# Kernel optimization log

Hardware: AMD Instinct MI355X
Metric: run time of the kernel (lower is better)

Reference implementation:

```python
import jax, jax.numpy as jnp
import numpy as np

HIDDEN = 4544
NUM_HEADS = 71
HEAD_DIM = 64
ROPE_BASE = 10000.0


def _rope_cos_sin(seq_len, dim, dtype):
    inv_freq = 1.0 / (ROPE_BASE ** (jnp.arange(0, dim, 2, dtype=jnp.float32) / dim))
    t = jnp.arange(seq_len, dtype=jnp.float32)
    freqs = jnp.einsum('i,j->ij', t, inv_freq)            # [S, dim/2]
    emb = jnp.concatenate([freqs, freqs], axis=-1)        # [S, dim]
    return jnp.cos(emb).astype(dtype), jnp.sin(emb).astype(dtype)


def _rotate_half(x):
    half = x.shape[-1] // 2
    return jnp.concatenate([-x[..., half:], x[..., :half]], axis=-1)


def _apply_rope(x, cos, sin):
    # x: [..., S, hd]; cos/sin: [S, hd]
    return x * cos + _rotate_half(x) * sin


def setup_inputs() -> dict:
    key = jax.random.key(0)
    k1, k2, k3 = jax.random.split(key, 3)
    B, S = 1, 1024
    hidden_states = jax.random.normal(k1, (B, 1, S, HIDDEN), dtype=jnp.float32) * 0.02
    # additive causal mask (prefill)
    neg = jnp.triu(jnp.full((S, S), -1e9, dtype=jnp.float32), k=1)
    attention_mask = jnp.broadcast_to(neg[None, None], (B, 1, S, S))
    # fused QKV weight (already transposed for right-matmul): [H, (nh+2)*hd]
    qkv_w = jax.random.normal(k2, (HIDDEN, (NUM_HEADS + 2) * HEAD_DIM), dtype=jnp.float32) * 0.02
    dense_w = jax.random.normal(k3, (HIDDEN, HIDDEN), dtype=jnp.float32) * 0.02
    return {"hidden_states": hidden_states, "attention_mask": attention_mask,
            "qkv_w": qkv_w, "dense_w": dense_w}


def reference(hidden_states, attention_mask, qkv_w, dense_w):
    B, _, S, H = hidden_states.shape
    nh, hd = NUM_HEADS, HEAD_DIM
    x = hidden_states[:, 0]                               # [B, S, H]
    fused = jnp.einsum('bsh,hf->bsf', x, qkv_w)           # [B, S, (nh+2)*hd]
    fused = fused.reshape(B, S, nh + 2, hd)
    q = jnp.transpose(fused[:, :, :nh, :], (0, 2, 1, 3))  # [B, nh, S, hd]
    k = fused[:, :, nh, :]                                # [B, S, hd]  (single KV head, MQA)
    v = fused[:, :, nh + 1, :]                            # [B, S, hd]
    cos, sin = _rope_cos_sin(S, hd, q.dtype)
    q = _apply_rope(q, cos, sin)
    k = _apply_rope(k, cos, sin)
    scale = 1.0 / np.sqrt(hd).astype(np.float32)
    scores = jnp.einsum('bhsd,btd->bhst', q, k) * scale   # [B, nh, S, S]
    scores = scores + attention_mask                      # broadcast over heads
    probs = jax.nn.softmax(scores, axis=-1)
    ctx = jnp.einsum('bhst,btd->bhsd', probs, v)          # [B, nh, S, hd]
    ctx = jnp.transpose(ctx, (0, 2, 1, 3)).reshape(B, S, nh * hd)
    out = jnp.einsum('bsh,hg->bsg', ctx, dense_w)         # [B, S, H]
    return out[:, None]                                   # [B, 1, S, H]
```

## Files before the change

### kernel.cpp

```cpp
#include <hip/hip_runtime.h>

#define S_LEN 1024
#define HID   4544
#define NH    71
#define NQKV  4672
#define NQKV_PAD 4736
#define ND_PAD   4608

typedef __attribute__((ext_vector_type(4)))  float f32x4;
typedef __attribute__((ext_vector_type(4))) unsigned short u16x4;
typedef __attribute__((ext_vector_type(8))) unsigned short u16x8;
typedef __attribute__((ext_vector_type(8))) __bf16 bf16x8;

__device__ __forceinline__ bf16x8 as_bf(u16x8 v) { return __builtin_bit_cast(bf16x8, v); }

__device__ __forceinline__ unsigned short f2bf(float f) {
    unsigned u = __builtin_bit_cast(unsigned, f);
    return (unsigned short)((u + 0x7FFFu + ((u >> 16) & 1u)) >> 16);
}
__device__ __forceinline__ float bf2f(unsigned short u) {
    return __builtin_bit_cast(float, (unsigned)u << 16);
}
__device__ __forceinline__ unsigned pk2(float a, float b) {
    return (unsigned)f2bf(a) | ((unsigned)f2bf(b) << 16);
}
__device__ __forceinline__ void gload16(const void* g, void* l) {
    __builtin_amdgcn_global_load_lds((const __attribute__((address_space(1))) unsigned int*)g,
                                     (__attribute__((address_space(3))) unsigned int*)l,
                                     16, 0, 0);
}

__global__ __launch_bounds__(256) void cvt_x_kernel(const float4* __restrict__ x,
                                                    ushort4* __restrict__ y) {
    int i = blockIdx.x * 256 + threadIdx.x;
    float4 v = x[i];
    ushort4 r;
    r.x = f2bf(v.x); r.y = f2bf(v.y); r.z = f2bf(v.z); r.w = f2bf(v.w);
    y[i] = r;
}

__global__ __launch_bounds__(256) void cvt_wT_kernel(const float* __restrict__ w,
                                                     unsigned short* __restrict__ wt,
                                                     int K, int N) {
    __shared__ float t[64][65];
    int n0 = blockIdx.x * 64, k0 = blockIdx.y * 64;
    int tx = threadIdx.x & 15, ty = threadIdx.x >> 4;
#pragma unroll
    for (int r = 0; r < 64; r += 16) {
        int k = k0 + ty + r;
        int n = n0 + tx * 4;
        float4 v = make_float4(0.f, 0.f, 0.f, 0.f);
        if (n < N) v = *(const float4*)&w[(size_t)k * N + n];
        t[ty + r][tx * 4 + 0] = v.x;
        t[ty + r][tx * 4 + 1] = v.y;
        t[ty + r][tx * 4 + 2] = v.z;
        t[ty + r][tx * 4 + 3] = v.w;
    }
    __syncthreads();
    int nr = threadIdx.x >> 2;
    int kq = (threadIdx.x & 3) * 16;
    unsigned short tmp[16];
#pragma unroll
    for (int z = 0; z < 16; z++) tmp[z] = f2bf(t[kq + z][nr]);
    u16x8* dst = (u16x8*)&wt[(size_t)(n0 + nr) * K + k0 + kq];
    dst[0] = *(const u16x8*)&tmp[0];
    dst[1] = *(const u16x8*)&tmp[8];
}

__global__ void rope_table_kernel(float* __restrict__ cs, float* __restrict__ sn) {
    int s = blockIdx.x, i = threadIdx.x;
    float inv = powf(10000.0f, -(2.0f * (float)i) / 64.0f);
    float f = (float)s * inv;
    cs[s * 32 + i] = cosf(f);
    sn[s * 32 + i] = sinf(f);
}

template<int EPI>
__global__ __launch_bounds__(128, 2) void gemm_bt_kernel(
        const unsigned short* __restrict__ A, const unsigned short* __restrict__ BT,
        void* __restrict__ Cout, const float* __restrict__ cs_t,
        const float* __restrict__ sn_t, unsigned short* __restrict__ k_out,
        unsigned short* __restrict__ v_out, int K, int ldc, int n_store) {
    __shared__ unsigned short As[2][64 * 64];
    __shared__ unsigned short Bs[2][128 * 64];
    int p = blockIdx.x;
    int per = gridDim.x >> 3;
    int l = (p & 7) * per + (p >> 3);
    int msl = l & 15, nb = l >> 4;
    int m0 = msl * 64, n0 = nb * 128;
    int t = threadIdx.x;
    int wn = t >> 6;
    int lane = t & 63, lr = lane & 15, lg = lane >> 4;

    f32x4 acc[4][4];
#pragma unroll
    for (int mi = 0; mi < 4; mi++)
#pragma unroll
        for (int ni = 0; ni < 4; ni++) acc[mi][ni] = (f32x4)0.0f;

    const char* Ab = (const char*)A;
    const char* Bb = (const char*)BT;
    size_t rs = (size_t)K * 2;

    auto stage = [&](int step, int buf) {
        size_t kb = (size_t)step * 128;
#pragma unroll
        for (int i = 0; i < 4; i++) {
            int chunk = i * 128 + t;
            int row = chunk >> 3, c8 = chunk & 7;
            int csrc = c8 ^ (row & 7);
            gload16(Ab + (size_t)(m0 + row) * rs + kb + csrc * 16,
                    (char*)As[buf] + chunk * 16);
        }
#pragma unroll
        for (int i = 0; i < 8; i++) {
            int chunk = i * 128 + t;
            int row = chunk >> 3, c8 = chunk & 7;
            int csrc = c8 ^ (row & 7);
            gload16(Bb + (size_t)(n0 + row) * rs + kb + csrc * 16,
                    (char*)Bs[buf] + chunk * 16);
        }
    };

    int nsteps = K >> 6;
    stage(0, 0);
    if (nsteps > 1) stage(1, 1);
    for (int s = 0; s < nsteps; ++s) {
        int cur = s & 1;
        if (s + 1 < nsteps) { asm volatile("s_waitcnt vmcnt(12)" ::: "memory"); }
        else                { asm volatile("s_waitcnt vmcnt(0)" ::: "memory"); }
        __builtin_amdgcn_s_barrier();
        bf16x8 af[4][2], bfr[4][2];
#pragma unroll
        for (int mi = 0; mi < 4; mi++) {
            int row = mi * 16 + lr;
#pragma unroll
            for (int kk = 0; kk < 2; kk++)
                af[mi][kk] = as_bf(*(const u16x8*)&As[cur][row * 64 + (((kk * 4 + lg) ^ (row & 7)) << 3)]);
        }
#pragma unroll
        for (int ni = 0; ni < 4; ni++) {
            int row = wn * 64 + ni * 16 + lr;
#pragma unroll
            for (int kk = 0; kk < 2; kk++)
                bfr[ni][kk] = as_bf(*(const u16x8*)&Bs[cur][row * 64 + (((kk * 4 + lg) ^ (row & 7)) << 3)]);
        }
        asm volatile("s_waitcnt lgkmcnt(0)" ::: "memory");
        __builtin_amdgcn_s_barrier();
        if (s + 2 < nsteps) stage(s + 2, cur);
#pragma unroll
        for (int kk = 0; kk < 2; kk++)
#pragma unroll
            for (int mi = 0; mi < 4; mi++)
#pragma unroll
                for (int ni = 0; ni < 4; ni++)
                    acc[mi][ni] = __builtin_amdgcn_mfma_f32_16x16x32_bf16(
                        af[mi][kk], bfr[ni][kk], acc[mi][ni], 0, 0, 0);
    }

    if (EPI == 0) {
        float* C = (float*)Cout;
#pragma unroll
        for (int mi = 0; mi < 4; mi++)
#pragma unroll
            for (int ni = 0; ni < 4; ni++) {
                int col = n0 + wn * 64 + ni * 16 + lr;
                if (col < n_store) {
#pragma unroll
                    for (int i = 0; i < 4; i++) {
                        int row = m0 + mi * 16 + 4 * lg + i;
                        C[(size_t)row * ldc + col] = acc[mi][ni][i];
                    }
                }
            }
    } else {
        int hh = nb * 2 + wn;
        if (hh == 72) {
#pragma unroll
            for (int mi = 0; mi < 4; mi++)
#pragma unroll
                for (int ni = 0; ni < 4; ni++) {
                    int d = ni * 16 + lr;
                    int s0 = m0 + mi * 16 + 4 * lg;
                    u16x4 pk;
#pragma unroll
                    for (int i = 0; i < 4; i++) pk[i] = f2bf(acc[mi][ni][i]);
                    *(u16x4*)&v_out[(size_t)d * S_LEN + s0] = pk;
                }
        } else if (hh < 72) {
            unsigned short* qb = (unsigned short*)Cout;
            float qscale = (hh < 71) ? 0.125f : 1.0f;
#pragma unroll
            for (int mi = 0; mi < 4; mi++)
#pragma unroll
                for (int i = 0; i < 4; i++) {
                    int s = m0 + mi * 16 + 4 * lg + i;
                    float c0 = cs_t[s * 32 + lr],      g0 = sn_t[s * 32 + lr];
                    float c1 = cs_t[s * 32 + 16 + lr], g1 = sn_t[s * 32 + 16 + lr];
#pragma unroll
                    for (int ni = 0; ni < 4; ni++) {
                        float x  = acc[mi][ni][i];
                        float xp = acc[mi][ni ^ 2][i];
                        float c = (ni & 1) ? c1 : c0;
                        float g = (ni & 1) ? g1 : g0;
                        float r = (ni < 2) ? (x * c - xp * g) : (x * c + xp * g);
                        r *= qscale;
                        int d = ni * 16 + lr;
                        if (hh < 71) qb[(size_t)s * HID + hh * 64 + d] = f2bf(r);
                        else         k_out[(size_t)s * 64 + d] = f2bf(r);
                    }
                }
        }
    }
}

__global__ __launch_bounds__(256, 3) void attn_kernel(
        const unsigned short* __restrict__ qb, const unsigned short* __restrict__ kr,
        const unsigned short* __restrict__ vt, unsigned short* __restrict__ ctx,
        unsigned short* __restrict__ Opart, float2* __restrict__ MLpart) {
    __shared__ unsigned short Ks[2][64 * 64];
    __shared__ unsigned short Vs[2][64 * 64];
    __shared__ unsigned short Pl[4][16 * 72];
    int h = blockIdx.y;
    int u = blockIdx.x;
    int c, j0;
    if (u < 16)      { c = 0; j0 = u * 4; }
    else if (u < 28) { c = 1; j0 = 16 + (u - 16) * 4; }
    else if (u < 36) { c = 2; j0 = 32 + (u - 28) * 4; }
    else             { c = 3; j0 = 48 + (u - 36) * 4; }
    int t = threadIdx.x, wv = t >> 6, lane = t & 63, lr = lane & 15, lg = lane >> 4;
    int j = j0 + wv;
    int qs = j * 16 + lr;
    int k_lo = c * 256;
    int kend_w   = min((j + 1) * 16, k_lo + 256);
    int kend_max = min((j0 + 4) * 16, k_lo + 256);
    int nt = (kend_max - k_lo) >> 6;
    int nch = (j >> 4) + 1;
    int srow = t >> 3, sc16 = t & 7, sw = lr & 7;

    auto stage = [&](int ti, int buf) {
        size_t kbase = (size_t)(k_lo + ti * 64);
#pragma unroll
        for (int i = 0; i < 2; i++) {
            int row = i * 32 + srow;
            int csrc = sc16 ^ (row & 7);
            gload16((const char*)kr + (kbase + row) * 128 + csrc * 16,
                    (char*)Ks[buf] + (i * 256 + t) * 16);
        }
#pragma unroll
        for (int i = 0; i < 2; i++) {
            int row = i * 32 + srow;
            int csrc = sc16 ^ (row & 7);
            gload16((const char*)vt + (size_t)row * 2048 + kbase * 2 + csrc * 16,
                    (char*)Vs[buf] + (i * 256 + t) * 16);
        }
    };

    bf16x8 qf[2];
#pragma unroll
    for (int dc = 0; dc < 2; dc++)
        qf[dc] = as_bf(*(const u16x8*)&qb[(size_t)qs * HID + h * 64 + dc * 32 + 8 * lg]);

    float m_i = -1e30f, l_i = 0.0f;
    f32x4 o[4];
#pragma unroll
    for (int d4 = 0; d4 < 4; d4++) o[d4] = (f32x4)0.0f;

    stage(0, 0);
    if (nt > 1) stage(1, 1);

    for (int ti = 0; ti < nt; ti++) {
        int cur = ti & 1;
        if (ti + 1 < nt) { asm volatile("s_waitcnt vmcnt(4)" ::: "memory"); }
        else             { asm volatile("s_waitcnt vmcnt(0)" ::: "memory"); }
        __builtin_amdgcn_s_barrier();
        int k0 = k_lo + ti * 64;
        if (k0 < kend_w) {
            f32x4 st[4];
#pragma unroll
            for (int nc = 0; nc < 4; nc++) st[nc] = (f32x4)0.0f;
#pragma unroll
            for (int nc = 0; nc < 4; nc++) {
                int krow = nc * 16 + lr;
#pragma unroll
                for (int dc = 0; dc < 2; dc++) {
                    bf16x8 kf = as_bf(*(const u16x8*)&Ks[cur][krow * 64 + (((dc * 4 + lg) ^ sw) << 3)]);
                    st[nc] = __builtin_amdgcn_mfma_f32_16x16x32_bf16(kf, qf[dc], st[nc], 0, 0, 0);
                }
            }
            bool needmask = (k0 + 64 > j * 16);
            float mx = -1e30f;
            if (needmask) {
#pragma unroll
                for (int nc = 0; nc < 4; nc++)
#pragma unroll
                    for (int i = 0; i < 4; i++) {
                        int ks = k0 + nc * 16 + 4 * lg + i;
                        float v = (ks <= qs) ? st[nc][i] : -1e30f;
                        st[nc][i] = v;
                        mx = fmaxf(mx, v);
                    }
            } else {
#pragma unroll
                for (int nc = 0; nc < 4; nc++)
#pragma unroll
                    for (int i = 0; i < 4; i++) mx = fmaxf(mx, st[nc][i]);
            }
            mx = fmaxf(mx, __shfl_xor(mx, 16));
            mx = fmaxf(mx, __shfl_xor(mx, 32));
            if (!__all(mx <= m_i + 8.0f)) {
                float mn = fmaxf(m_i, mx);
                float so = __expf(m_i - mn);
                l_i *= so;
#pragma unroll
                for (int d4 = 0; d4 < 4; d4++)
#pragma unroll
                    for (int i = 0; i < 4; i++) o[d4][i] *= so;
                m_i = mn;
            }
            float ps = 0.0f;
#pragma unroll
            for (int nc = 0; nc < 4; nc++)
#pragma unroll
                for (int i = 0; i < 4; i++) {
                    float v = st[nc][i];
                    float e = (!needmask || v > -1e29f) ? __expf(v - m_i) : 0.0f;
                    st[nc][i] = e;
                    ps += e;
                }
            ps += __shfl_xor(ps, 16);
            ps += __shfl_xor(ps, 32);
            l_i += ps;
#pragma unroll
            for (int nc = 0; nc < 4; nc++) {
                *(unsigned*)&Pl[wv][lr * 72 + nc * 16 + 4 * lg]     = pk2(st[nc][0], st[nc][1]);
                *(unsigned*)&Pl[wv][lr * 72 + nc * 16 + 4 * lg + 2] = pk2(st[nc][2], st[nc][3]);
            }
            bf16x8 pb[2];
#pragma unroll
            for (int kk = 0; kk < 2; kk++)
                pb[kk] = as_bf(*(const u16x8*)&Pl[wv][lr * 72 + kk * 32 + 8 * lg]);
#pragma unroll
            for (int d4 = 0; d4 < 4; d4++) {
                int vrow = d4 * 16 + lr;
#pragma unroll
                for (int kk = 0; kk < 2; kk++) {
                    bf16x8 vf = as_bf(*(const u16x8*)&Vs[cur][vrow * 64 + (((kk * 4 + lg) ^ sw) << 3)]);
                    o[d4] = __builtin_amdgcn_mfma_f32_16x16x32_bf16(vf, pb[kk], o[d4], 0, 0, 0);
                }
            }
        }
        __builtin_amdgcn_s_barrier();
        if (ti + 2 < nt) stage(ti + 2, cur);
    }

    if (nch == 1) {
        float linv = 1.0f / l_i;
#pragma unroll
        for (int d4 = 0; d4 < 4; d4++) {
            u16x4 pk;
#pragma unroll
            for (int i = 0; i < 4; i++) pk[i] = f2bf(o[d4][i] * linv);
            *(u16x4*)&ctx[(size_t)qs * HID + h * 64 + d4 * 16 + 4 * lg] = pk;
        }
    } else {
        int pi = (h * 48 + (j - 16)) * 4 + c;
#pragma unroll
        for (int d4 = 0; d4 < 4; d4++) {
            u16x4 pk;
#pragma unroll
            for (int i = 0; i < 4; i++) pk[i] = f2bf(o[d4][i]);
            *(u16x4*)&Opart[(size_t)pi * 1024 + lr * 64 + d4 * 16 + 4 * lg] = pk;
        }
        if (lg == 0) MLpart[pi * 16 + lr] = make_float2(m_i, l_i);
    }
}

__global__ __launch_bounds__(256) void merge_kernel(
        const unsigned short* __restrict__ Opart, const float2* __restrict__ MLpart,
        unsigned short* __restrict__ ctx) {
    int mu = blockIdx.x * 4 + (threadIdx.x >> 6);
    int lane = threadIdx.x & 63;
    int h = mu / 48, jj = mu % 48, j = 16 + jj;
    int nch = (j >> 4) + 1;
    int base = (h * 48 + jj) * 4;
    for (int q = 0; q < 16; q++) {
        float m[4], l[4], w[4];
        float M = -1e30f;
        for (int c = 0; c < nch; c++) {
            float2 ml = MLpart[(base + c) * 16 + q];
            m[c] = ml.x; l[c] = ml.y;
            M = fmaxf(M, m[c]);
        }
        float L = 0.0f;
        for (int c = 0; c < nch; c++) { w[c] = __expf(m[c] - M); L += l[c] * w[c]; }
        float acc = 0.0f;
        for (int c = 0; c < nch; c++)
            acc += w[c] * bf2f(Opart[(size_t)(base + c) * 1024 + q * 64 + lane]);
        ctx[(size_t)(j * 16 + q) * HID + h * 64 + lane] = f2bf(acc / L);
    }
}

extern "C" void kernel_launch(void* const* d_in, const int* in_sizes, int n_in,
                              void* d_out, int out_size, void* d_ws, size_t ws_size,
                              hipStream_t stream) {
    const float* hs      = (const float*)d_in[0];
    const float* qkv_w   = (const float*)d_in[2];
    const float* dense_w = (const float*)d_in[3];
    float* out = (float*)d_out;

    char* ws = (char*)d_ws;
    size_t off = 0;
    auto alloc = [&](size_t bytes) -> void* {
        void* p = ws + off;
        off += (bytes + 255) & ~(size_t)255;
        return p;
    };
    unsigned short* x_bf   = (unsigned short*)alloc((size_t)S_LEN * HID * 2);
    unsigned short* wqkvT  = (unsigned short*)alloc((size_t)NQKV_PAD * HID * 2);
    unsigned short* q_bf   = (unsigned short*)alloc((size_t)S_LEN * HID * 2);
    unsigned short* k_rope = (unsigned short*)alloc((size_t)S_LEN * 64 * 2);
    unsigned short* v_t    = (unsigned short*)alloc((size_t)64 * S_LEN * 2);
    unsigned short* ctx    = (unsigned short*)alloc((size_t)S_LEN * HID * 2);
    unsigned short* wdT    = (unsigned short*)alloc((size_t)ND_PAD * HID * 2);
    float*          cs_t   = (float*)alloc((size_t)S_LEN * 32 * 4);
    float*          sn_t   = (float*)alloc((size_t)S_LEN * 32 * 4);
    (void)ws_size;
    unsigned short* Opart  = wqkvT;
    float2*         MLpart = (float2*)((char*)wqkvT + (size_t)71 * 48 * 4 * 1024 * 2);

    cvt_x_kernel<<<dim3(S_LEN * HID / 1024), dim3(256), 0, stream>>>(
        (const float4*)hs, (ushort4*)x_bf);
    cvt_wT_kernel<<<dim3(NQKV_PAD / 64, HID / 64), dim3(256), 0, stream>>>(
        qkv_w, wqkvT, HID, NQKV);
    cvt_wT_kernel<<<dim3(ND_PAD / 64, HID / 64), dim3(256), 0, stream>>>(
        dense_w, wdT, HID, HID);
    rope_table_kernel<<<dim3(S_LEN), dim3(32), 0, stream>>>(cs_t, sn_t);

    gemm_bt_kernel<1><<<dim3(16 * NQKV_PAD / 128), dim3(128), 0, stream>>>(
        x_bf, wqkvT, q_bf, cs_t, sn_t, k_rope, v_t, HID, HID, NQKV);

    attn_kernel<<<dim3(40, NH), dim3(256), 0, stream>>>(
        q_bf, k_rope, v_t, ctx, Opart, MLpart);

    merge_kernel<<<dim3(NH * 48 / 4), dim3(256), 0, stream>>>(Opart, MLpart, ctx);

    gemm_bt_kernel<0><<<dim3(16 * ND_PAD / 128), dim3(128), 0, stream>>>(
        ctx, wdT, out, nullptr, nullptr, nullptr, nullptr, HID, HID, HID);
}
```

Measured before the change: 259.2 us.

## Fuse prep kernels and overlap dense-weight conversion with QKV GEMM

Merges the input conversion, QKV weight transpose and RoPE table kernels into one prep launch. The dense-weight transpose/convert is moved into extra blocks of the QKV GEMM launch so it can run alongside GEMM tiles. This removes launch overhead and serialization between small kernels. In exchange the GEMM kernel's shared memory becomes a unified buffer, and the extra transpose blocks compete with GEMM blocks for CUs.

Measured after the change: 251.9 us. 1.03x faster.

```diff
diff --git a/kernel.cpp b/kernel.cpp
--- a/kernel.cpp
+++ b/kernel.cpp
@@ -7,6 +7,10 @@
 #define NQKV_PAD 4736
 #define ND_PAD   4608
 
+#define XB (S_LEN * HID / 1024)
+#define WB ((NQKV_PAD / 64) * (HID / 64))
+#define RB 128
+
 typedef __attribute__((ext_vector_type(4)))  float f32x4;
 typedef __attribute__((ext_vector_type(4))) unsigned short u16x4;
 typedef __attribute__((ext_vector_type(8))) unsigned short u16x8;
@@ -30,49 +34,48 @@
                                      16, 0, 0);
 }
 
-__global__ __launch_bounds__(256) void cvt_x_kernel(const float4* __restrict__ x,
-                                                    ushort4* __restrict__ y) {
-    int i = blockIdx.x * 256 + threadIdx.x;
-    float4 v = x[i];
-    ushort4 r;
-    r.x = f2bf(v.x); r.y = f2bf(v.y); r.z = f2bf(v.z); r.w = f2bf(v.w);
-    y[i] = r;
-}
-
-__global__ __launch_bounds__(256) void cvt_wT_kernel(const float* __restrict__ w,
-                                                     unsigned short* __restrict__ wt,
-                                                     int K, int N) {
-    __shared__ float t[64][65];
-    int n0 = blockIdx.x * 64, k0 = blockIdx.y * 64;
-    int tx = threadIdx.x & 15, ty = threadIdx.x >> 4;
-#pragma unroll
-    for (int r = 0; r < 64; r += 16) {
-        int k = k0 + ty + r;
-        int n = n0 + tx * 4;
-        float4 v = make_float4(0.f, 0.f, 0.f, 0.f);
-        if (n < N) v = *(const float4*)&w[(size_t)k * N + n];
-        t[ty + r][tx * 4 + 0] = v.x;
-        t[ty + r][tx * 4 + 1] = v.y;
-        t[ty + r][tx * 4 + 2] = v.z;
-        t[ty + r][tx * 4 + 3] = v.w;
-    }
-    __syncthreads();
-    int nr = threadIdx.x >> 2;
-    int kq = (threadIdx.x & 3) * 16;
-    unsigned short tmp[16];
-#pragma unroll
-    for (int z = 0; z < 16; z++) tmp[z] = f2bf(t[kq + z][nr]);
-    u16x8* dst = (u16x8*)&wt[(size_t)(n0 + nr) * K + k0 + kq];
-    dst[0] = *(const u16x8*)&tmp[0];
-    dst[1] = *(const u16x8*)&tmp[8];
-}
-
-__global__ void rope_table_kernel(float* __restrict__ cs, float* __restrict__ sn) {
-    int s = blockIdx.x, i = threadIdx.x;
-    float inv = powf(10000.0f, -(2.0f * (float)i) / 64.0f);
-    float f = (float)s * inv;
-    cs[s * 32 + i] = cosf(f);
-    sn[s * 32 + i] = sinf(f);
+__global__ __launch_bounds__(256) void prep_kernel(
+        const float4* __restrict__ x, ushort4* __restrict__ y,
+        const float* __restrict__ qkv_w, unsigned short* __restrict__ wqkvT,
+        float* __restrict__ cs, float* __restrict__ sn) {
+    __shared__ float tb[64][65];
+    int bx = blockIdx.x, t = threadIdx.x;
+    if (bx < XB) {
+        int i = bx * 256 + t;
+        float4 v = x[i];
+        ushort4 r;
+        r.x = f2bf(v.x); r.y = f2bf(v.y); r.z = f2bf(v.z); r.w = f2bf(v.w);
+        y[i] = r;
+    } else if (bx < XB + WB) {
+        int idx = bx - XB;
+        int n0 = (idx % (NQKV_PAD / 64)) * 64, k0 = (idx / (NQKV_PAD / 64)) * 64;
+        int tx = t & 15, ty = t >> 4;
+#pragma unroll
+        for (int r = 0; r < 64; r += 16) {
+            int k = k0 + ty + r, n = n0 + tx * 4;
+            float4 v = make_float4(0.f, 0.f, 0.f, 0.f);
+            if (n < NQKV) v = *(const float4*)&qkv_w[(size_t)k * NQKV + n];
+            tb[ty + r][tx * 4 + 0] = v.x;
+            tb[ty + r][tx * 4 + 1] = v.y;
+            tb[ty + r][tx * 4 + 2] = v.z;
+            tb[ty + r][tx * 4 + 3] = v.w;
+        }
+        __syncthreads();
+        int nr = t >> 2, kq = (t & 3) * 16;
+        unsigned short tmp[16];
+#pragma unroll
+        for (int z = 0; z < 16; z++) tmp[z] = f2bf(tb[kq + z][nr]);
+        u16x8* dst = (u16x8*)&wqkvT[(size_t)(n0 + nr) * HID + k0 + kq];
+        dst[0] = *(const u16x8*)&tmp[0];
+        dst[1] = *(const u16x8*)&tmp[8];
+    } else {
+        int gi = (bx - XB - WB) * 256 + t;
+        int s = gi >> 5, i = gi & 31;
+        float inv = powf(10000.0f, -(2.0f * (float)i) / 64.0f);
+        float f = (float)s * inv;
+        cs[s * 32 + i] = cosf(f);
+        sn[s * 32 + i] = sinf(f);
+    }
 }
 
 template<int EPI>
@@ -80,15 +83,47 @@
         const unsigned short* __restrict__ A, const unsigned short* __restrict__ BT,
         void* __restrict__ Cout, const float* __restrict__ cs_t,
         const float* __restrict__ sn_t, unsigned short* __restrict__ k_out,
-        unsigned short* __restrict__ v_out, int K, int ldc, int n_store) {
-    __shared__ unsigned short As[2][64 * 64];
-    __shared__ unsigned short Bs[2][128 * 64];
+        unsigned short* __restrict__ v_out, int K, int ldc, int n_store,
+        const float* __restrict__ w2, unsigned short* __restrict__ wt2,
+        int gemm_blocks) {
+    __shared__ char smem[49152];
+    unsigned short* As0 = (unsigned short*)smem;
+    unsigned short* Bs0 = (unsigned short*)(smem + 16384);
+    int t = threadIdx.x;
+
+    if ((int)blockIdx.x >= gemm_blocks) {
+        float (*tb)[65] = (float(*)[65])smem;
+        int idx = (int)blockIdx.x - gemm_blocks;
+        int n0 = (idx % (ND_PAD / 64)) * 64, k0 = (idx / (ND_PAD / 64)) * 64;
+        int tx = t & 15, ty = t >> 4;
+#pragma unroll
+        for (int r = 0; r < 64; r += 8) {
+            int k = k0 + ty + r, n = n0 + tx * 4;
+            float4 v = make_float4(0.f, 0.f, 0.f, 0.f);
+            if (n < HID) v = *(const float4*)&w2[(size_t)k * HID + n];
+            tb[ty + r][tx * 4 + 0] = v.x;
+            tb[ty + r][tx * 4 + 1] = v.y;
+            tb[ty + r][tx * 4 + 2] = v.z;
+            tb[ty + r][tx * 4 + 3] = v.w;
+        }
+        __syncthreads();
+        int nr = t >> 1, kh = (t & 1) * 32;
+        unsigned short tmp[32];
+#pragma unroll
+        for (int z = 0; z < 32; z++) tmp[z] = f2bf(tb[kh + z][nr]);
+        u16x8* dst = (u16x8*)&wt2[(size_t)(n0 + nr) * HID + k0 + kh];
+        dst[0] = *(const u16x8*)&tmp[0];
+        dst[1] = *(const u16x8*)&tmp[8];
+        dst[2] = *(const u16x8*)&tmp[16];
+        dst[3] = *(const u16x8*)&tmp[24];
+        return;
+    }
+
     int p = blockIdx.x;
-    int per = gridDim.x >> 3;
+    int per = gemm_blocks >> 3;
     int l = (p & 7) * per + (p >> 3);
     int msl = l & 15, nb = l >> 4;
     int m0 = msl * 64, n0 = nb * 128;
-    int t = threadIdx.x;
     int wn = t >> 6;
     int lane = t & 63, lr = lane & 15, lg = lane >> 4;
 
@@ -110,7 +145,7 @@
             int row = chunk >> 3, c8 = chunk & 7;
             int csrc = c8 ^ (row & 7);
             gload16(Ab + (size_t)(m0 + row) * rs + kb + csrc * 16,
-                    (char*)As[buf] + chunk * 16);
+                    (char*)As0 + buf * 8192 + chunk * 16);
         }
 #pragma unroll
         for (int i = 0; i < 8; i++) {
@@ -118,7 +153,7 @@
             int row = chunk >> 3, c8 = chunk & 7;
             int csrc = c8 ^ (row & 7);
             gload16(Bb + (size_t)(n0 + row) * rs + kb + csrc * 16,
-                    (char*)Bs[buf] + chunk * 16);
+                    (char*)Bs0 + buf * 16384 + chunk * 16);
         }
     };
 
@@ -136,14 +171,14 @@
             int row = mi * 16 + lr;
 #pragma unroll
             for (int kk = 0; kk < 2; kk++)
-                af[mi][kk] = as_bf(*(const u16x8*)&As[cur][row * 64 + (((kk * 4 + lg) ^ (row & 7)) << 3)]);
+                af[mi][kk] = as_bf(*(const u16x8*)&As0[cur * 4096 + row * 64 + (((kk * 4 + lg) ^ (row & 7)) << 3)]);
         }
 #pragma unroll
         for (int ni = 0; ni < 4; ni++) {
             int row = wn * 64 + ni * 16 + lr;
 #pragma unroll
             for (int kk = 0; kk < 2; kk++)
-                bfr[ni][kk] = as_bf(*(const u16x8*)&Bs[cur][row * 64 + (((kk * 4 + lg) ^ (row & 7)) << 3)]);
+                bfr[ni][kk] = as_bf(*(const u16x8*)&Bs0[cur * 8192 + row * 64 + (((kk * 4 + lg) ^ (row & 7)) << 3)]);
         }
         asm volatile("s_waitcnt lgkmcnt(0)" ::: "memory");
         __builtin_amdgcn_s_barrier();
@@ -429,22 +464,19 @@
     unsigned short* Opart  = wqkvT;
     float2*         MLpart = (float2*)((char*)wqkvT + (size_t)71 * 48 * 4 * 1024 * 2);
 
-    cvt_x_kernel<<<dim3(S_LEN * HID / 1024), dim3(256), 0, stream>>>(
-        (const float4*)hs, (ushort4*)x_bf);
-    cvt_wT_kernel<<<dim3(NQKV_PAD / 64, HID / 64), dim3(256), 0, stream>>>(
-        qkv_w, wqkvT, HID, NQKV);
-    cvt_wT_kernel<<<dim3(ND_PAD / 64, HID / 64), dim3(256), 0, stream>>>(
-        dense_w, wdT, HID, HID);
-    rope_table_kernel<<<dim3(S_LEN), dim3(32), 0, stream>>>(cs_t, sn_t);
-
-    gemm_bt_kernel<1><<<dim3(16 * NQKV_PAD / 128), dim3(128), 0, stream>>>(
-        x_bf, wqkvT, q_bf, cs_t, sn_t, k_rope, v_t, HID, HID, NQKV);
+    prep_kernel<<<dim3(XB + WB + RB), dim3(256), 0, stream>>>(
+        (const float4*)hs, (ushort4*)x_bf, qkv_w, wqkvT, cs_t, sn_t);
+
+    gemm_bt_kernel<1><<<dim3(592 + (ND_PAD / 64) * (HID / 64)), dim3(128), 0, stream>>>(
+        x_bf, wqkvT, q_bf, cs_t, sn_t, k_rope, v_t, HID, HID, NQKV,
+        dense_w, wdT, 592);
 
     attn_kernel<<<dim3(40, NH), dim3(256), 0, stream>>>(
         q_bf, k_rope, v_t, ctx, Opart, MLpart);
 
     merge_kernel<<<dim3(NH * 48 / 4), dim3(256), 0, stream>>>(Opart, MLpart, ctx);
 
-    gemm_bt_kernel<0><<<dim3(16 * ND_PAD / 128), dim3(128), 0, stream>>>(
-        ctx, wdT, out, nullptr, nullptr, nullptr, nullptr, HID, HID, HID);
-}
+    gemm_bt_kernel<0><<<dim3(576), dim3(128), 0, stream>>>(
+        ctx, wdT, out, nullptr, nullptr, nullptr, nullptr, HID, HID, HID,
+        nullptr, nullptr, 576);
+}
```
